# Kernel tuning notes

Measured on AMD Instinct MI355X. Metric: run time of the kernel, lower is better.

Reference implementation:

```python
import jax, jax.numpy as jnp
import numpy as np

B, L1, L2, D = 16, 512, 512, 512
H, INNER = 8, 1024
HD = INNER // H  # 128

def _glorot(key, shape):
    fan_in, fan_out = shape[-2], shape[-1]
    lim = jnp.sqrt(6.0 / (fan_in + fan_out))
    return jax.random.uniform(key, shape, jnp.float32, -lim, lim)

def setup_inputs() -> dict:
    key = jax.random.key(0)
    ks = jax.random.split(key, 8)
    return {
        "primary": jax.random.normal(ks[0], (B, L1, D), jnp.float32),
        "secondary": jax.random.normal(ks[1], (B, L2, D), jnp.float32),
        "primary_mask": jnp.ones((B, L1), jnp.float32),
        "secondary_mask": jnp.ones((B, L2), jnp.float32),
        "W_aff": _glorot(ks[2], (H, D, D)),          # per-head bilinear affinity weights
        "W_p": _glorot(ks[3], (D, INNER)),            # linear_primary (no bias)
        "W_s": _glorot(ks[4], (D, INNER)),            # linear_secondary (no bias)
        "W_fp": _glorot(ks[5], (D + HD, D)),          # ffn_primary
        "b_fp": jnp.zeros((D,), jnp.float32),
        "W_fs": _glorot(ks[6], (D + HD, D)),          # ffn_secondary
        "b_fs": jnp.zeros((D,), jnp.float32),
    }

def reference(primary, secondary, primary_mask, secondary_mask,
              W_aff, W_p, W_s, W_fp, b_fp, W_fs, b_fs):
    b, l1, d = primary.shape
    l2 = secondary.shape[1]
    h = W_aff.shape[0]
    hd = W_p.shape[1] // h
    # affinity mask: (B, 1, L1, L2)
    mask = (primary_mask[:, :, None] * secondary_mask[:, None, :])[:, None, :, :]
    # multi-head bilinear affinity: tanh(P Wk S^T) -> (B, H, L1, L2)
    aff = jnp.tanh(jnp.einsum('bie,hef,bjf->bhij', primary, W_aff, secondary)) * mask
    # project + split heads -> (B, H, L, hd)
    pp = (primary @ W_p).reshape(b, l1, h, hd).transpose(0, 2, 1, 3)
    ps = (secondary @ W_s).reshape(b, l2, h, hd).transpose(0, 2, 1, 3)
    # weighted sums (ReLU activation)
    wp = jax.nn.relu(jnp.einsum('bhij,bhid->bhjd', aff, pp))  # (B, H, L2, hd)
    ws = jax.nn.relu(jnp.einsum('bhij,bhjd->bhid', aff, ps))  # (B, H, L1, hd)
    # GlobalMaxPool1D applied to (L, H, hd) per sample => max over heads
    pool_p = wp.max(axis=1)  # (B, L2, hd)
    pool_s = ws.max(axis=1)  # (B, L1, hd)
    out_p = jax.nn.relu(jnp.concatenate([primary, pool_s], -1) @ W_fp + b_fp)
    out_s = jax.nn.relu(jnp.concatenate([secondary, pool_p], -1) @ W_fs + b_fs)
    return out_p, out_s
```

## Files before the change

kernel.cpp:

```cpp
#include <hip/hip_runtime.h>
#include <hip/hip_bf16.h>

typedef short short8 __attribute__((ext_vector_type(8)));
typedef float f32x16 __attribute__((ext_vector_type(16)));
typedef float f32x4 __attribute__((ext_vector_type(4)));

#define BM 128
#define BN 128

typedef const __attribute__((address_space(1))) void gas_t;
typedef __attribute__((address_space(3))) void las_t;

__device__ __forceinline__ unsigned short f2bf(float f) {
  unsigned int u = __float_as_uint(f);
  u += 0x7FFFu + ((u >> 16) & 1u);
  return (unsigned short)(u >> 16);
}

__device__ __forceinline__ float fast_tanh(float x) {
  x = fminf(fmaxf(x, -10.f), 10.f);
  float t = __builtin_amdgcn_exp2f(x * 2.8853900817779268f);
  return 1.f - 2.f * __builtin_amdgcn_rcpf(t + 1.f);
}

struct GemmP {
  const unsigned short* A;
  const unsigned short* Bm;
  void* C;
  const float* A2f;
  const unsigned short* A_b;
  const unsigned short* Bm_b;
  void* C_b;
  const float* A2f_b;
  const float* mask_p;
  const float* mask_s;
  const float* bias;
  const float* bias_b;
  long long sAb, sAh, sBb, sBh, sCb, sCh;
  int lda, lda2, ldb, ldc, M, N, K, Hh, kSplit, zSplit, nbx, nby;
};

template <int TA, int EPI>
__device__ __forceinline__ void gemm_body(const GemmP& p, int bx, int by, int bz, char* smem_) {
  constexpr int PA = (TA == 0) ? 32 : 40;
  constexpr int HSA = (TA == 0) ? 4096 : 5120;
  unsigned short* As = (unsigned short*)smem_;
  unsigned short* Bs = (unsigned short*)(smem_ + 2 * HSA * 2);

  int z = bz;
  const unsigned short* Abase = p.A;
  const unsigned short* Bbase = p.Bm;
  void* Cvp = p.C;
  const float* A2f = p.A2f;
  const float* bias = p.bias;
  if (p.zSplit && z >= p.zSplit) {
    z -= p.zSplit;
    Abase = p.A_b; Bbase = p.Bm_b; Cvp = p.C_b; A2f = p.A2f_b; bias = p.bias_b;
  }
  const int zb = z / p.Hh, zh = z % p.Hh;
  const unsigned short* A = Abase + (size_t)zb * p.sAb + (size_t)zh * p.sAh;
  const unsigned short* B = Bbase + (size_t)zb * p.sBb + (size_t)zh * p.sBh;
  const int m0 = bx * BM, n0 = by * BN;
  const int tid = threadIdx.x;
  const int wid = tid >> 6, lane = tid & 63;
  const int wm = (wid >> 1) * 64, wn = (wid & 1) * 64;
  const int lrow = lane & 31;
  const int lk8 = (lane >> 5) * 8;

  f32x16 acc[2][2] = {};

  const int dm = tid >> 2, dkg = tid & 3;

  auto mfma_block = [&]() {
#pragma unroll
    for (int h = 0; h < 2; ++h)
#pragma unroll
      for (int kc = 0; kc < 2; ++kc) {
        short8 af[2], bfv[2];
#pragma unroll
        for (int mt = 0; mt < 2; ++mt)
          af[mt] = *(const short8*)&As[h * HSA + (wm + mt * 32 + lrow) * PA + kc * 16 + lk8];
#pragma unroll
        for (int nt = 0; nt < 2; ++nt)
          bfv[nt] = *(const short8*)&Bs[h * 4096 + (wn + nt * 32 + lrow) * 32 + kc * 16 + lk8];
#pragma unroll
        for (int mt = 0; mt < 2; ++mt)
#pragma unroll
          for (int nt = 0; nt < 2; ++nt)
            acc[mt][nt] = __builtin_amdgcn_mfma_f32_32x32x16_bf16(af[mt], bfv[nt], acc[mt][nt], 0, 0, 0);
      }
  };
  auto stage_b = [&](int k0) {
#pragma unroll
    for (int h = 0; h < 2; ++h)
#pragma unroll
      for (int q = 0; q < 2; ++q) {
        const unsigned short* src = B + (size_t)(n0 + q * 64 + dm) * p.ldb + (k0 + h * 32 + dkg * 8);
        __builtin_amdgcn_global_load_lds((gas_t*)src,
                                         (las_t*)&Bs[h * 4096 + q * 2048 + wid * 512],
                                         16, 0, 0);
      }
  };

  const int nIter = p.K >> 6;
  const int nIter1 = p.kSplit ? (p.kSplit >> 6) : nIter;

  for (int it = 0; it < nIter1; ++it) {
    const int k0 = it << 6;
    if (TA == 0) {
#pragma unroll
      for (int h = 0; h < 2; ++h)
#pragma unroll
        for (int q = 0; q < 2; ++q) {
          const unsigned short* src = A + (size_t)(m0 + q * 64 + dm) * p.lda + (k0 + h * 32 + dkg * 8);
          __builtin_amdgcn_global_load_lds((gas_t*)src,
                                           (las_t*)&As[h * HSA + q * 2048 + wid * 512],
                                           16, 0, 0);
        }
    } else {
      const int kk = tid & 31, mg = (tid >> 5) << 4;
#pragma unroll
      for (int h = 0; h < 2; ++h) {
        const unsigned short* src = A + (size_t)(k0 + h * 32 + kk) * p.lda + (m0 + mg);
        uint4 v0 = *(const uint4*)src;
        uint4 v1 = *(const uint4*)(src + 8);
        unsigned short tmp[16];
        *(uint4*)&tmp[0] = v0;
        *(uint4*)&tmp[8] = v1;
#pragma unroll
        for (int j = 0; j < 16; ++j) As[h * HSA + (mg + j) * PA + kk] = tmp[j];
      }
    }
    stage_b(k0);
    __syncthreads();
    mfma_block();
    __syncthreads();
  }

  if (TA == 0 && p.kSplit) {
    for (int it = nIter1; it < nIter; ++it) {
      const int k0 = it << 6;
#pragma unroll
      for (int h = 0; h < 2; ++h) {
        const int ko = k0 + h * 32 - p.kSplit;
#pragma unroll
        for (int q = 0; q < 2; ++q) {
          const float* src = A2f + (size_t)(m0 + q * 64 + dm) * p.lda2 + (ko + dkg * 8);
          float4 v0 = *(const float4*)src;
          float4 v1 = *(const float4*)(src + 4);
          __attribute__((aligned(16))) unsigned short t[8];
          t[0] = f2bf(v0.x); t[1] = f2bf(v0.y); t[2] = f2bf(v0.z); t[3] = f2bf(v0.w);
          t[4] = f2bf(v1.x); t[5] = f2bf(v1.y); t[6] = f2bf(v1.z); t[7] = f2bf(v1.w);
          *(uint4*)&As[h * HSA + (q * 64 + dm) * 32 + dkg * 8] = *(const uint4*)t;
        }
      }
      stage_b(k0);
      __syncthreads();
      mfma_block();
      __syncthreads();
    }
  }

  unsigned short* Cu = (unsigned short*)Cvp + (size_t)zb * p.sCb + (size_t)zh * p.sCh;
  float* Cf = (float*)Cvp + (size_t)zb * p.sCb + (size_t)zh * p.sCh;

  const int rbase = 4 * (lane >> 5);

  float mp[2][16], ms[2];
  if constexpr (EPI == 1) {
#pragma unroll
    for (int mt = 0; mt < 2; ++mt)
#pragma unroll
      for (int reg = 0; reg < 16; ++reg) {
        const int rl = (reg & 3) + 8 * (reg >> 2) + rbase;
        mp[mt][reg] = p.mask_p[(size_t)zb * p.M + (m0 + wm + mt * 32 + rl)];
      }
#pragma unroll
    for (int nt = 0; nt < 2; ++nt)
      ms[nt] = p.mask_s[(size_t)zb * p.N + (n0 + wn + nt * 32 + lrow)];
  }
  if constexpr (EPI == 3) {
#pragma unroll
    for (int nt = 0; nt < 2; ++nt)
      ms[nt] = bias[n0 + wn + nt * 32 + lrow];
  }

#pragma unroll
  for (int mt = 0; mt < 2; ++mt) {
#pragma unroll
    for (int nt = 0; nt < 2; ++nt) {
      f32x16 a = acc[mt][nt];
#pragma unroll
      for (int reg = 0; reg < 16; ++reg) {
        const int rl = (reg & 3) + 8 * (reg >> 2) + rbase;
        const int grow = m0 + wm + mt * 32 + rl;
        const int gcol = n0 + wn + nt * 32 + lrow;
        const size_t idx = (size_t)grow * p.ldc + gcol;
        const float v = a[reg];
        if constexpr (EPI == 0) {
          Cu[idx] = f2bf(v);
        } else if constexpr (EPI == 1) {
          Cu[idx] = f2bf(fast_tanh(v) * (mp[mt][reg] * ms[nt]));
        } else if constexpr (EPI == 2) {
          atomicMax((int*)Cf + idx, __float_as_int(fmaxf(v, 0.f)));
        } else {
          Cf[idx] = fmaxf(v + ms[nt], 0.f);
        }
      }
    }
  }
}

template <int TA, int EPI>
__global__ __launch_bounds__(256) void gemm_k(GemmP p) {
  extern __shared__ char smem[];
  gemm_body<TA, EPI>(p, blockIdx.x, blockIdx.y, blockIdx.z, smem);
}

template <int TA1, int EPI1, int TA2, int EPI2>
__global__ __launch_bounds__(256) void gemm_pair_k(GemmP a, GemmP b, int nA) {
  extern __shared__ char smem[];
  int bid = blockIdx.x;
  if (bid < nA) {
    const int per = a.nbx * a.nby;
    const int z = bid / per, r = bid % per;
    gemm_body<TA1, EPI1>(a, r % a.nbx, r / a.nbx, z, smem);
  } else {
    bid -= nA;
    const int per = b.nbx * b.nby;
    const int z = bid / per, r = bid % per;
    gemm_body<TA2, EPI2>(b, r % b.nbx, r / b.nbx, z, smem);
  }
}

#define VMW0() asm volatile("s_waitcnt vmcnt(0)" ::: "memory")

template <int EPI>
__device__ __forceinline__ void gemm10_body(const GemmP& p, int bx, int by, int bz, char* smem_) {
  int z = bz;
  const unsigned short* Abase = p.A;
  const unsigned short* Bbase = p.Bm;
  void* Cvp = p.C;
  if (p.zSplit && z >= p.zSplit) {
    z -= p.zSplit;
    Abase = p.A_b; Bbase = p.Bm_b; Cvp = p.C_b;
  }
  const int zb = z / p.Hh, zh = z % p.Hh;
  const unsigned short* A = Abase + (size_t)zb * p.sAb + (size_t)zh * p.sAh;
  const unsigned short* B = Bbase + (size_t)zb * p.sBb + (size_t)zh * p.sBh;
  const int m0 = bx * 256, n0 = by * 256;
  const int tid = threadIdx.x;
  const int wid = tid >> 6, lane = tid & 63;
  const int wm = wid >> 2, wn = wid & 3;
  const int lrow = lane & 15, lhi = lane >> 4;

  const int rr = tid >> 3;
  const int cs = ((tid & 7) * 8) ^ ((rr & 7) << 3);

  const int colx = (lhi * 16) ^ ((lrow & 7) << 4);
  const int offA = (wm * 128 + lrow) * 128 + colx;
  const int offB = 32768 + (wn * 64 + lrow) * 128 + colx;

  f32x4 acc[8][4] = {};

  auto stageA = [&](int t, int slot) {
    const int k0 = t << 6;
    const unsigned short* s0 = A + (size_t)(m0 + rr) * p.lda + k0 + cs;
#pragma unroll
    for (int s = 0; s < 4; ++s)
      __builtin_amdgcn_global_load_lds((gas_t*)(s0 + (size_t)(s * 64) * p.lda),
                                       (las_t*)(smem_ + slot * 65536 + s * 8192 + tid * 16),
                                       16, 0, 0);
  };
  auto stageB = [&](int t, int slot) {
    const int k0 = t << 6;
    const unsigned short* s0 = B + (size_t)(n0 + rr) * p.ldb + k0 + cs;
#pragma unroll
    for (int s = 0; s < 4; ++s)
      __builtin_amdgcn_global_load_lds((gas_t*)(s0 + (size_t)(s * 64) * p.ldb),
                                       (las_t*)(smem_ + slot * 65536 + 32768 + s * 8192 + tid * 16),
                                       16, 0, 0);
  };

  const int nt = p.K >> 6;

  stageA(0, 0); stageB(0, 0);
  VMW0();
  __builtin_amdgcn_s_barrier();
  __builtin_amdgcn_sched_barrier(0);

  for (int t = 0; t < nt; ++t) {
    const int slot = t & 1, other = slot ^ 1;
    const char* sb = smem_ + slot * 65536;
    short8 af[4], bv[4];

#pragma unroll
    for (int fn = 0; fn < 4; ++fn) bv[fn] = *(const short8*)(sb + offB + fn * 2048);
#pragma unroll
    for (int fm = 0; fm < 4; ++fm) af[fm] = *(const short8*)(sb + offA + fm * 2048);
    if (t + 1 < nt) stageA(t + 1, other);
    __builtin_amdgcn_s_setprio(1);
#pragma unroll
    for (int fm = 0; fm < 4; ++fm)
#pragma unroll
      for (int fn = 0; fn < 4; ++fn)
        acc[fm][fn] = __builtin_amdgcn_mfma_f32_16x16x32_bf16(af[fm], bv[fn], acc[fm][fn], 0, 0, 0);
    __builtin_amdgcn_s_setprio(0);

#pragma unroll
    for (int fm = 0; fm < 4; ++fm) af[fm] = *(const short8*)(sb + offA + (4 + fm) * 2048);
    if (t + 1 < nt) stageB(t + 1, other);
    __builtin_amdgcn_s_setprio(1);
#pragma unroll
    for (int fm = 0; fm < 4; ++fm)
#pragma unroll
      for (int fn = 0; fn < 4; ++fn)
        acc[4 + fm][fn] = __builtin_amdgcn_mfma_f32_16x16x32_bf16(af[fm], bv[fn], acc[4 + fm][fn], 0, 0, 0);
    __builtin_amdgcn_s_setprio(0);

#pragma unroll
    for (int fn = 0; fn < 4; ++fn) bv[fn] = *(const short8*)(sb + (offB ^ 64) + fn * 2048);
#pragma unroll
    for (int fm = 0; fm < 4; ++fm) af[fm] = *(const short8*)(sb + (offA ^ 64) + fm * 2048);
    __builtin_amdgcn_s_setprio(1);
#pragma unroll
    for (int fm = 0; fm < 4; ++fm)
#pragma unroll
      for (int fn = 0; fn < 4; ++fn)
        acc[fm][fn] = __builtin_amdgcn_mfma_f32_16x16x32_bf16(af[fm], bv[fn], acc[fm][fn], 0, 0, 0);
    __builtin_amdgcn_s_setprio(0);

#pragma unroll
    for (int fm = 0; fm < 4; ++fm) af[fm] = *(const short8*)(sb + (offA ^ 64) + (4 + fm) * 2048);
    __builtin_amdgcn_s_setprio(1);
#pragma unroll
    for (int fm = 0; fm < 4; ++fm)
#pragma unroll
      for (int fn = 0; fn < 4; ++fn)
        acc[4 + fm][fn] = __builtin_amdgcn_mfma_f32_16x16x32_bf16(af[fm], bv[fn], acc[4 + fm][fn], 0, 0, 0);
    __builtin_amdgcn_s_setprio(0);

    if (t + 1 < nt) {
      VMW0();
      __builtin_amdgcn_s_barrier();
      __builtin_amdgcn_sched_barrier(0);
    }
  }

  unsigned short* Cu = (unsigned short*)Cvp + (size_t)zb * p.sCb + (size_t)zh * p.sCh;

  float ms[4];
  if constexpr (EPI == 1) {
#pragma unroll
    for (int fn = 0; fn < 4; ++fn)
      ms[fn] = p.mask_s[(size_t)zb * p.N + (n0 + wn * 64 + fn * 16 + lrow)];
  }

#pragma unroll
  for (int fm = 0; fm < 8; ++fm)
#pragma unroll
    for (int fn = 0; fn < 4; ++fn) {
      f32x4 a = acc[fm][fn];
      const int gcol = n0 + wn * 64 + fn * 16 + lrow;
#pragma unroll
      for (int reg = 0; reg < 4; ++reg) {
        const int grow = m0 + wm * 128 + fm * 16 + lhi * 4 + reg;
        const size_t idx = (size_t)grow * p.ldc + gcol;
        if constexpr (EPI == 0) {
          Cu[idx] = f2bf(a[reg]);
        } else {
          const float mp = p.mask_p[(size_t)zb * p.M + grow];
          Cu[idx] = f2bf(fast_tanh(a[reg]) * (mp * ms[fn]));
        }
      }
    }
}

template <int EPI>
__global__ __launch_bounds__(512, 1) void gemm10_k(GemmP p) {
  extern __shared__ char smem[];
  gemm10_body<EPI>(p, blockIdx.x, blockIdx.y, blockIdx.z, smem);
}

template <int E1, int E2>
__global__ __launch_bounds__(512, 1) void gemm10_pair_k(GemmP a, GemmP b, int nA) {
  extern __shared__ char smem[];
  int bid = blockIdx.x;
  if (bid < nA) {
    const int per = a.nbx * a.nby;
    const int z = bid / per, r = bid % per;
    gemm10_body<E1>(a, r % a.nbx, r / a.nbx, z, smem);
  } else {
    bid -= nA;
    const int per = b.nbx * b.nby;
    const int z = bid / per, r = bid % per;
    gemm10_body<E2>(b, r % b.nbx, r / b.nbx, z, smem);
  }
}

__device__ __forceinline__ void trans_body(const float* src, unsigned short* dst,
                                           int R, int C, int bx, int by, float (*tile)[33]) {
  const int r0 = by * 32, c0 = bx * 32;
  const int tx = threadIdx.x & 31, ty = threadIdx.x >> 5;
#pragma unroll
  for (int j = 0; j < 4; ++j)
    tile[ty + j * 8][tx] = src[(size_t)(r0 + ty + j * 8) * C + (c0 + tx)];
  __syncthreads();
#pragma unroll
  for (int j = 0; j < 4; ++j)
    dst[(size_t)(c0 + ty + j * 8) * R + (r0 + tx)] = f2bf(tile[tx][ty + j * 8]);
}

__global__ __launch_bounds__(256) void prep_k(const float* P, const float* S,
                                              unsigned short* Pbf, unsigned short* Sbf,
                                              const float* W_aff, unsigned short* WaT,
                                              const float* W_p, unsigned short* WpT,
                                              const float* W_s, unsigned short* WsT,
                                              const float* W_fp, unsigned short* WfpT,
                                              const float* W_fs, unsigned short* WfsT,
                                              float* poolz) {
  __shared__ float tile[32][33];
  const int bid = blockIdx.x;
  if (bid < 8192) {
    const int n4 = 1048576;
    int i = bid * 256 + threadIdx.x;
    const float4* s = (const float4*)P;
    ushort4* d = (ushort4*)Pbf;
    if (i >= n4) { i -= n4; s = (const float4*)S; d = (ushort4*)Sbf; }
    float4 v = s[i];
    ushort4 o;
    o.x = f2bf(v.x); o.y = f2bf(v.y); o.z = f2bf(v.z); o.w = f2bf(v.w);
    d[i] = o;
  } else if (bid < 10240) {
    const int l = bid - 8192;
    const int z = l >> 8, r = l & 255;
    trans_body(W_aff + (size_t)z * 262144, WaT + (size_t)z * 262144, 512, 512,
               r & 15, r >> 4, tile);
  } else if (bid < 11264) {
    const int l = bid - 10240;
    const int z = l >> 9, r = l & 511;
    trans_body(z ? W_s : W_p, z ? WsT : WpT, 512, 1024, r & 31, r >> 5, tile);
  } else if (bid < 11904) {
    const int l = bid - 11264;
    const int z = l / 320, r = l % 320;
    trans_body(z ? W_fs : W_fp, z ? WfsT : WfpT, 640, 512, r & 15, r >> 4, tile);
  } else {
    const int i = (bid - 11904) * 256 + threadIdx.x;
    ((float4*)poolz)[i] = float4{0.f, 0.f, 0.f, 0.f};
  }
}

extern "C" void kernel_launch(void* const* d_in, const int* in_sizes, int n_in,
                              void* d_out, int out_size, void* d_ws, size_t ws_size,
                              hipStream_t stream) {
  (void)in_sizes; (void)n_in; (void)out_size; (void)ws_size;
  const float* primary   = (const float*)d_in[0];
  const float* secondary = (const float*)d_in[1];
  const float* pmask     = (const float*)d_in[2];
  const float* smask     = (const float*)d_in[3];
  const float* W_aff     = (const float*)d_in[4];
  const float* W_p       = (const float*)d_in[5];
  const float* W_s       = (const float*)d_in[6];
  const float* W_fp      = (const float*)d_in[7];
  const float* b_fp      = (const float*)d_in[8];
  const float* W_fs      = (const float*)d_in[9];
  const float* b_fs      = (const float*)d_in[10];

  constexpr int Bb = 16, L = 512, Dd = 512, Hh = 8, HDd = 128, INNER = 1024, CAT = 640;
  constexpr int NT = Hh * Dd;
  constexpr long long LD = (long long)L * Dd;
  constexpr long long LL = (long long)L * L;

  static bool s_attr = [] {
    hipFuncSetAttribute(reinterpret_cast<const void*>(&gemm10_pair_k<0, 0>),
                        hipFuncAttributeMaxDynamicSharedMemorySize, 131072);
    hipFuncSetAttribute(reinterpret_cast<const void*>(&gemm10_k<1>),
                        hipFuncAttributeMaxDynamicSharedMemorySize, 131072);
    return true;
  }();
  (void)s_attr;

  char* base = (char*)d_ws;
  size_t off = 0;
  auto alloc = [&](size_t bytes) -> void* {
    void* r = base + off;
    off += (bytes + 255) & ~(size_t)255;
    return r;
  };

  unsigned short* Pbf   = (unsigned short*)alloc((size_t)Bb * L * Dd * 2);
  unsigned short* Sbf   = (unsigned short*)alloc((size_t)Bb * L * Dd * 2);
  unsigned short* WaT   = (unsigned short*)alloc((size_t)NT * Dd * 2);
  unsigned short* WpT   = (unsigned short*)alloc((size_t)INNER * Dd * 2);
  unsigned short* WsT   = (unsigned short*)alloc((size_t)INNER * Dd * 2);
  unsigned short* WfpT  = (unsigned short*)alloc((size_t)Dd * CAT * 2);
  unsigned short* WfsT  = (unsigned short*)alloc((size_t)Dd * CAT * 2);
  unsigned short* psT   = (unsigned short*)alloc((size_t)Bb * INNER * L * 2);
  unsigned short* ppT   = (unsigned short*)alloc((size_t)Bb * INNER * L * 2);
  unsigned short* Tbuf  = (unsigned short*)alloc((size_t)Bb * L * NT * 2);
  unsigned short* affb  = (unsigned short*)alloc((size_t)Bb * Hh * L * L * 2);
  float* pool_p = (float*)alloc((size_t)Bb * L * HDd * 4);
  float* pool_s = (float*)alloc((size_t)Bb * L * HDd * 4);

  prep_k<<<dim3(13952), dim3(256), 0, stream>>>(primary, secondary, Pbf, Sbf,
                                                W_aff, WaT, W_p, WpT, W_s, WsT,
                                                W_fp, WfpT, W_fs, WfsT, pool_p);

  {
    GemmP a{};
    a.A = Pbf; a.lda = Dd;
    a.Bm = WaT; a.ldb = Dd;
    a.C = Tbuf; a.ldc = NT;
    a.M = Bb * L; a.N = NT; a.K = Dd; a.Hh = 1; a.nbx = 32; a.nby = 16;

    GemmP b{};
    b.A = WsT; b.lda = Dd; b.sAb = 0;
    b.Bm = Sbf; b.ldb = Dd; b.sBb = LD;
    b.C = psT; b.ldc = L; b.sCb = (long long)INNER * L;
    b.A_b = WpT; b.Bm_b = Pbf; b.C_b = ppT;
    b.M = INNER; b.N = L; b.K = Dd; b.Hh = 1; b.zSplit = Bb; b.nbx = 4; b.nby = 2;

    gemm10_pair_k<0, 0><<<dim3(512 + 256), dim3(512), 131072, stream>>>(a, b, 512);
  }

  {
    GemmP g{};
    g.A = Tbuf; g.lda = NT; g.sAb = (long long)L * NT; g.sAh = Dd;
    g.Bm = Sbf; g.ldb = Dd; g.sBb = LD; g.sBh = 0;
    g.C = affb; g.ldc = L; g.sCb = (long long)Hh * LL; g.sCh = LL;
    g.mask_p = pmask; g.mask_s = smask;
    g.M = L; g.N = L; g.K = Dd; g.Hh = Hh;
    gemm10_k<1><<<dim3(2, 2, Bb * Hh), dim3(512), 131072, stream>>>(g);
  }

  {
    GemmP g4{};
    g4.A = affb; g4.lda = L; g4.sAb = (long long)Hh * LL; g4.sAh = LL;
    g4.Bm = psT; g4.ldb = L; g4.sBb = (long long)INNER * L; g4.sBh = (long long)HDd * L;
    g4.C = pool_s; g4.ldc = HDd; g4.sCb = (long long)L * HDd; g4.sCh = 0;
    g4.M = L; g4.N = HDd; g4.K = L; g4.Hh = Hh; g4.nbx = 4; g4.nby = 1;

    GemmP g5 = g4;
    g5.Bm = ppT;
    g5.C = pool_p;

    gemm_pair_k<0, 2, 1, 2><<<dim3(512 + 512), dim3(256), 36864, stream>>>(g4, g5, 512);
  }

  {
    GemmP g{};
    g.A = Pbf; g.lda = Dd;
    g.A2f = pool_s; g.lda2 = HDd; g.kSplit = Dd;
    g.Bm = WfpT; g.ldb = CAT;
    g.C = d_out; g.ldc = Dd;
    g.bias = b_fp;
    g.A_b = Sbf; g.A2f_b = pool_p; g.Bm_b = WfsT;
    g.C_b = (float*)d_out + (size_t)Bb * L * Dd;
    g.bias_b = b_fs;
    g.M = Bb * L; g.N = Dd; g.K = CAT; g.Hh = 1; g.zSplit = 1;
    gemm_k<0, 3><<<dim3(64, 4, 2), dim3(256), 32768, stream>>>(g);
  }
}
```

Measured before the change: 316.7 us.

## Switch big GEMMs to 256x128 single-buffered tiles with two blocks per CU

```diff
diff --git a/kernel.cpp b/kernel.cpp
--- a/kernel.cpp
+++ b/kernel.cpp
@@ -233,10 +233,8 @@
   }
 }
 
-#define VMW0() asm volatile("s_waitcnt vmcnt(0)" ::: "memory")
-
 template <int EPI>
-__device__ __forceinline__ void gemm10_body(const GemmP& p, int bx, int by, int bz, char* smem_) {
+__device__ __forceinline__ void gemm11_body(const GemmP& p, int bx, int by, int bz, char* smem_) {
   int z = bz;
   const unsigned short* Abase = p.A;
   const unsigned short* Bbase = p.Bm;
@@ -248,10 +246,10 @@
   const int zb = z / p.Hh, zh = z % p.Hh;
   const unsigned short* A = Abase + (size_t)zb * p.sAb + (size_t)zh * p.sAh;
   const unsigned short* B = Bbase + (size_t)zb * p.sBb + (size_t)zh * p.sBh;
-  const int m0 = bx * 256, n0 = by * 256;
+  const int m0 = bx * 256, n0 = by * 128;
   const int tid = threadIdx.x;
   const int wid = tid >> 6, lane = tid & 63;
-  const int wm = wid >> 2, wn = wid & 3;
+  const int wm = wid >> 1, wn = wid & 1;
   const int lrow = lane & 15, lhi = lane >> 4;
 
   const int rr = tid >> 3;
@@ -263,42 +261,27 @@
 
   f32x4 acc[8][4] = {};
 
-  auto stageA = [&](int t, int slot) {
+  const int nt = p.K >> 6;
+
+  for (int t = 0; t < nt; ++t) {
     const int k0 = t << 6;
-    const unsigned short* s0 = A + (size_t)(m0 + rr) * p.lda + k0 + cs;
+    const unsigned short* sa = A + (size_t)(m0 + rr) * p.lda + k0 + cs;
+#pragma unroll
+    for (int s = 0; s < 8; ++s)
+      __builtin_amdgcn_global_load_lds((gas_t*)(sa + (size_t)(s * 32) * p.lda),
+                                       (las_t*)(smem_ + s * 4096 + tid * 16), 16, 0, 0);
+    const unsigned short* sb = B + (size_t)(n0 + rr) * p.ldb + k0 + cs;
 #pragma unroll
     for (int s = 0; s < 4; ++s)
-      __builtin_amdgcn_global_load_lds((gas_t*)(s0 + (size_t)(s * 64) * p.lda),
-                                       (las_t*)(smem_ + slot * 65536 + s * 8192 + tid * 16),
-                                       16, 0, 0);
-  };
-  auto stageB = [&](int t, int slot) {
-    const int k0 = t << 6;
-    const unsigned short* s0 = B + (size_t)(n0 + rr) * p.ldb + k0 + cs;
-#pragma unroll
-    for (int s = 0; s < 4; ++s)
-      __builtin_amdgcn_global_load_lds((gas_t*)(s0 + (size_t)(s * 64) * p.ldb),
-                                       (las_t*)(smem_ + slot * 65536 + 32768 + s * 8192 + tid * 16),
-                                       16, 0, 0);
-  };
-
-  const int nt = p.K >> 6;
-
-  stageA(0, 0); stageB(0, 0);
-  VMW0();
-  __builtin_amdgcn_s_barrier();
-  __builtin_amdgcn_sched_barrier(0);
-
-  for (int t = 0; t < nt; ++t) {
-    const int slot = t & 1, other = slot ^ 1;
-    const char* sb = smem_ + slot * 65536;
+      __builtin_amdgcn_global_load_lds((gas_t*)(sb + (size_t)(s * 32) * p.ldb),
+                                       (las_t*)(smem_ + 32768 + s * 4096 + tid * 16), 16, 0, 0);
+    __syncthreads();
+
     short8 af[4], bv[4];
-
-#pragma unroll
-    for (int fn = 0; fn < 4; ++fn) bv[fn] = *(const short8*)(sb + offB + fn * 2048);
-#pragma unroll
-    for (int fm = 0; fm < 4; ++fm) af[fm] = *(const short8*)(sb + offA + fm * 2048);
-    if (t + 1 < nt) stageA(t + 1, other);
+#pragma unroll
+    for (int fn = 0; fn < 4; ++fn) bv[fn] = *(const short8*)(smem_ + offB + fn * 2048);
+#pragma unroll
+    for (int fm = 0; fm < 4; ++fm) af[fm] = *(const short8*)(smem_ + offA + fm * 2048);
     __builtin_amdgcn_s_setprio(1);
 #pragma unroll
     for (int fm = 0; fm < 4; ++fm)
@@ -308,8 +291,7 @@
     __builtin_amdgcn_s_setprio(0);
 
 #pragma unroll
-    for (int fm = 0; fm < 4; ++fm) af[fm] = *(const short8*)(sb + offA + (4 + fm) * 2048);
-    if (t + 1 < nt) stageB(t + 1, other);
+    for (int fm = 0; fm < 4; ++fm) af[fm] = *(const short8*)(smem_ + offA + (4 + fm) * 2048);
     __builtin_amdgcn_s_setprio(1);
 #pragma unroll
     for (int fm = 0; fm < 4; ++fm)
@@ -319,9 +301,9 @@
     __builtin_amdgcn_s_setprio(0);
 
 #pragma unroll
-    for (int fn = 0; fn < 4; ++fn) bv[fn] = *(const short8*)(sb + (offB ^ 64) + fn * 2048);
-#pragma unroll
-    for (int fm = 0; fm < 4; ++fm) af[fm] = *(const short8*)(sb + (offA ^ 64) + fm * 2048);
+    for (int fn = 0; fn < 4; ++fn) bv[fn] = *(const short8*)(smem_ + (offB ^ 64) + fn * 2048);
+#pragma unroll
+    for (int fm = 0; fm < 4; ++fm) af[fm] = *(const short8*)(smem_ + (offA ^ 64) + fm * 2048);
     __builtin_amdgcn_s_setprio(1);
 #pragma unroll
     for (int fm = 0; fm < 4; ++fm)
@@ -331,7 +313,7 @@
     __builtin_amdgcn_s_setprio(0);
 
 #pragma unroll
-    for (int fm = 0; fm < 4; ++fm) af[fm] = *(const short8*)(sb + (offA ^ 64) + (4 + fm) * 2048);
+    for (int fm = 0; fm < 4; ++fm) af[fm] = *(const short8*)(smem_ + (offA ^ 64) + (4 + fm) * 2048);
     __builtin_amdgcn_s_setprio(1);
 #pragma unroll
     for (int fm = 0; fm < 4; ++fm)
@@ -340,11 +322,7 @@
         acc[4 + fm][fn] = __builtin_amdgcn_mfma_f32_16x16x32_bf16(af[fm], bv[fn], acc[4 + fm][fn], 0, 0, 0);
     __builtin_amdgcn_s_setprio(0);
 
-    if (t + 1 < nt) {
-      VMW0();
-      __builtin_amdgcn_s_barrier();
-      __builtin_amdgcn_sched_barrier(0);
-    }
+    if (t + 1 < nt) __syncthreads();
   }
 
   unsigned short* Cu = (unsigned short*)Cvp + (size_t)zb * p.sCb + (size_t)zh * p.sCh;
@@ -377,24 +355,24 @@
 }
 
 template <int EPI>
-__global__ __launch_bounds__(512, 1) void gemm10_k(GemmP p) {
+__global__ __launch_bounds__(256, 2) void gemm11_k(GemmP p) {
   extern __shared__ char smem[];
-  gemm10_body<EPI>(p, blockIdx.x, blockIdx.y, blockIdx.z, smem);
+  gemm11_body<EPI>(p, blockIdx.x, blockIdx.y, blockIdx.z, smem);
 }
 
 template <int E1, int E2>
-__global__ __launch_bounds__(512, 1) void gemm10_pair_k(GemmP a, GemmP b, int nA) {
+__global__ __launch_bounds__(256, 2) void gemm11_pair_k(GemmP a, GemmP b, int nA) {
   extern __shared__ char smem[];
   int bid = blockIdx.x;
   if (bid < nA) {
     const int per = a.nbx * a.nby;
     const int z = bid / per, r = bid % per;
-    gemm10_body<E1>(a, r % a.nbx, r / a.nbx, z, smem);
+    gemm11_body<E1>(a, r % a.nbx, r / a.nbx, z, smem);
   } else {
     bid -= nA;
     const int per = b.nbx * b.nby;
     const int z = bid / per, r = bid % per;
-    gemm10_body<E2>(b, r % b.nbx, r / b.nbx, z, smem);
+    gemm11_body<E2>(b, r % b.nbx, r / b.nbx, z, smem);
   }
 }
 
@@ -472,10 +450,10 @@
   constexpr long long LL = (long long)L * L;
 
   static bool s_attr = [] {
-    hipFuncSetAttribute(reinterpret_cast<const void*>(&gemm10_pair_k<0, 0>),
-                        hipFuncAttributeMaxDynamicSharedMemorySize, 131072);
-    hipFuncSetAttribute(reinterpret_cast<const void*>(&gemm10_k<1>),
-                        hipFuncAttributeMaxDynamicSharedMemorySize, 131072);
+    hipFuncSetAttribute(reinterpret_cast<const void*>(&gemm11_pair_k<0, 0>),
+                        hipFuncAttributeMaxDynamicSharedMemorySize, 49152);
+    hipFuncSetAttribute(reinterpret_cast<const void*>(&gemm11_k<1>),
+                        hipFuncAttributeMaxDynamicSharedMemorySize, 49152);
     return true;
   }();
   (void)s_attr;
@@ -511,16 +489,16 @@
     a.A = Pbf; a.lda = Dd;
     a.Bm = WaT; a.ldb = Dd;
     a.C = Tbuf; a.ldc = NT;
-    a.M = Bb * L; a.N = NT; a.K = Dd; a.Hh = 1; a.nbx = 32; a.nby = 16;
+    a.M = Bb * L; a.N = NT; a.K = Dd; a.Hh = 1; a.nbx = 32; a.nby = 32;
 
     GemmP b{};
     b.A = WsT; b.lda = Dd; b.sAb = 0;
     b.Bm = Sbf; b.ldb = Dd; b.sBb = LD;
     b.C = psT; b.ldc = L; b.sCb = (long long)INNER * L;
     b.A_b = WpT; b.Bm_b = Pbf; b.C_b = ppT;
-    b.M = INNER; b.N = L; b.K = Dd; b.Hh = 1; b.zSplit = Bb; b.nbx = 4; b.nby = 2;
-
-    gemm10_pair_k<0, 0><<<dim3(512 + 256), dim3(512), 131072, stream>>>(a, b, 512);
+    b.M = INNER; b.N = L; b.K = Dd; b.Hh = 1; b.zSplit = Bb; b.nbx = 4; b.nby = 4;
+
+    gemm11_pair_k<0, 0><<<dim3(1024 + 512), dim3(256), 49152, stream>>>(a, b, 1024);
   }
 
   {
@@ -530,7 +508,7 @@
     g.C = affb; g.ldc = L; g.sCb = (long long)Hh * LL; g.sCh = LL;
     g.mask_p = pmask; g.mask_s = smask;
     g.M = L; g.N = L; g.K = Dd; g.Hh = Hh;
-    gemm10_k<1><<<dim3(2, 2, Bb * Hh), dim3(512), 131072, stream>>>(g);
+    gemm11_k<1><<<dim3(2, 4, Bb * Hh), dim3(256), 49152, stream>>>(g);
   }
 
   {
```

After: 322.4 us. No clear change (+1.8%).
